# Kernel optimization log

Measured on AMD Instinct MI355X. Metric: run time of the kernel, lower is better.

Reference implementation:

```python
import jax, jax.numpy as jnp
import numpy as np

N_ATOMS = 4096
N_ANGLES = 200000


def setup_inputs() -> dict:
    key = jax.random.key(0)
    k1, k2, k3, k4, k5 = jax.random.split(key, 5)
    # pairwise unit direction vectors [N, N, 3]
    vec = jax.random.normal(k1, (N_ATOMS, N_ATOMS, 3), dtype=jnp.float32)
    vec = vec / jnp.linalg.norm(vec, axis=-1, keepdims=True)
    # pairwise distances [N, N], strictly positive
    dist = jax.random.uniform(k2, (N_ATOMS, N_ATOMS), dtype=jnp.float32) * 2.0 + 0.5
    # angle triplets [A, 3]
    coord_idx = jax.random.randint(k3, (N_ANGLES, 3), 0, N_ATOMS)
    # per-angle parameters: k0 (force const) and theta0 (equilibrium angle, rad)
    k0 = jax.random.uniform(k4, (N_ANGLES,), dtype=jnp.float32) * 100.0
    theta0 = jax.random.uniform(k5, (N_ANGLES,), dtype=jnp.float32) * np.float32(np.pi)
    params = jnp.stack([k0, theta0], axis=1)
    forces_out = jnp.zeros((N_ATOMS, 3), dtype=jnp.float32)
    return {
        "dist_mat": dist,
        "vector_mat": vec,
        "forces_out": forces_out,
        "params": params,
        "coord_idx": coord_idx,
        "calc_energy": 1,
        "calc_forces": 1,
    }


def reference(dist_mat, vector_mat, forces_out, params, coord_idx, calc_energy, calc_forces):
    k0 = params[:, 0]
    theta0 = params[:, 1]
    a1 = coord_idx[:, 0]
    a2 = coord_idx[:, 1]
    a3 = coord_idx[:, 2]

    vec21 = vector_mat[a2, a1]            # [A, 3]
    vec23 = vector_mat[a2, a3]            # [A, 3]
    dist21 = dist_mat[a2, a1]             # [A]
    dist23 = dist_mat[a2, a3]             # [A]

    cos_theta = jnp.clip(jnp.sum(vec21 * vec23, axis=1), -1.0, 1.0)
    theta = jnp.arccos(cos_theta)
    delta_theta = theta - theta0

    if calc_energy:
        energy = jnp.sum(k0 * delta_theta * delta_theta)
    else:
        energy = jnp.zeros([1], dtype=forces_out.dtype)

    forces = forces_out
    if calc_forces:
        sin_theta = jnp.sqrt(1.0 - cos_theta * cos_theta)
        # matches torch nan_to_num(nan=0.0): zero out coef where sin_theta == 0
        coef = jnp.where(sin_theta > 0.0,
                         -2.0 * k0 * delta_theta / jnp.maximum(sin_theta, 1e-12),
                         0.0)
        force0 = coef[:, None] * (cos_theta[:, None] * vec21 - vec23) / dist21[:, None]
        force2 = coef[:, None] * (cos_theta[:, None] * vec23 - vec21) / dist23[:, None]
        force1 = -(force0 + force2)
        forces = forces.at[a1].add(force0).at[a2].add(force1).at[a3].add(force2)

    return energy, forces
```

## Files before the change

kernel.cpp:

```cpp
#include <hip/hip_runtime.h>


__global__ void init_out_kernel(float* __restrict__ out,
                                const float* __restrict__ forces0,
                                int nf) {
    int j = blockIdx.x * blockDim.x + threadIdx.x;
    if (j == 0) out[0] = 0.0f;
    if (j < nf) out[1 + j] = forces0[j];
}

#define NB 256
#define NT 1024

__global__ void __launch_bounds__(NT)
angle_fused_kernel(const float*  __restrict__ dist,
                   const float*  __restrict__ vec,
                   const float2* __restrict__ params,
                   const int*    __restrict__ cidx,
                   const int*    __restrict__ ce_p,
                   const int*    __restrict__ cf_p,
                   float* __restrict__ out,
                   int n_atoms, int n_angles) {
    extern __shared__ float s_f[];
    __shared__ float s_e;
    const int nf  = n_atoms * 3;
    const int tid = threadIdx.x;
    const int b   = blockIdx.x;

    for (int j = tid; j < nf; j += NT) s_f[j] = 0.0f;
    if (tid == 0) s_e = 0.0f;
    __syncthreads();

    const int ce = ce_p[0];
    const int cf = cf_p[0];

    const int i0 = (int)(((long)b * n_angles) / NB);
    const int i1 = (int)(((long)(b + 1) * n_angles) / NB);
    const int i  = i0 + tid;

    float e_acc = 0.0f;
    if (i < i1) {
        const int a1 = cidx[3 * i + 0];
        const int a2 = cidx[3 * i + 1];
        const int a3 = cidx[3 * i + 2];
        const float2 kt = params[i];

        const unsigned row = (unsigned)a2 * (unsigned)n_atoms;
        const unsigned b21 = row + (unsigned)a1;
        const unsigned b23 = row + (unsigned)a3;
        const float* __restrict__ p21 = vec + 3u * b21;
        const float* __restrict__ p23 = vec + 3u * b23;

        const float v21x = p21[0], v21y = p21[1], v21z = p21[2];
        const float v23x = p23[0], v23y = p23[1], v23z = p23[2];
        const float d21 = dist[b21];
        const float d23 = dist[b23];

        float c = v21x * v23x + v21y * v23y + v21z * v23z;
        c = fminf(1.0f, fmaxf(-1.0f, c));
        const float th  = acosf(c);
        const float dth = th - kt.y;

        if (ce) e_acc = kt.x * dth * dth;

        if (cf) {
            const float s2 = fmaxf(0.0f, 1.0f - c * c);
            const float s  = sqrtf(s2);
            const float coef = (s > 0.0f) ? (-2.0f * kt.x * dth / fmaxf(s, 1e-12f)) : 0.0f;
            const float i21 = coef / d21;
            const float i23 = coef / d23;

            const float f0x = i21 * (c * v21x - v23x);
            const float f0y = i21 * (c * v21y - v23y);
            const float f0z = i21 * (c * v21z - v23z);
            const float f2x = i23 * (c * v23x - v21x);
            const float f2y = i23 * (c * v23y - v21y);
            const float f2z = i23 * (c * v23z - v21z);

            atomicAdd(&s_f[a1 * 3 + 0], f0x);
            atomicAdd(&s_f[a1 * 3 + 1], f0y);
            atomicAdd(&s_f[a1 * 3 + 2], f0z);
            atomicAdd(&s_f[a2 * 3 + 0], -(f0x + f2x));
            atomicAdd(&s_f[a2 * 3 + 1], -(f0y + f2y));
            atomicAdd(&s_f[a2 * 3 + 2], -(f0z + f2z));
            atomicAdd(&s_f[a3 * 3 + 0], f2x);
            atomicAdd(&s_f[a3 * 3 + 1], f2y);
            atomicAdd(&s_f[a3 * 3 + 2], f2z);
        }
    }

    for (int off = 32; off > 0; off >>= 1)
        e_acc += __shfl_down(e_acc, off, 64);
    if ((tid & 63) == 0) atomicAdd(&s_e, e_acc);
    __syncthreads();

    if (ce && tid == 0) atomicAdd(&out[0], s_e);

    if (cf) {
        const int base = (b * (nf / NB)) % nf;
        for (int jj = tid; jj < nf; jj += NT) {
            int j = jj + base;
            if (j >= nf) j -= nf;
            const float v = s_f[j];
            if (v != 0.0f) atomicAdd(&out[1 + j], v);
        }
    }
}

extern "C" void kernel_launch(void* const* d_in, const int* in_sizes, int n_in,
                              void* d_out, int out_size, void* d_ws, size_t ws_size,
                              hipStream_t stream) {
    const float*  dist    = (const float*)d_in[0];
    const float*  vec     = (const float*)d_in[1];
    const float*  forces0 = (const float*)d_in[2];
    const float2* params  = (const float2*)d_in[3];
    const int*    cidx    = (const int*)d_in[4];
    const int*    ce_p    = (const int*)d_in[5];
    const int*    cf_p    = (const int*)d_in[6];
    float* out = (float*)d_out;

    const int n_atoms  = in_sizes[2] / 3;
    const int n_angles = in_sizes[4] / 3;
    const int nf = n_atoms * 3;

    init_out_kernel<<<(nf + 1 + 255) / 256, 256, 0, stream>>>(out, forces0, nf);

    const size_t lds_bytes = (size_t)nf * sizeof(float);
    angle_fused_kernel<<<NB, NT, lds_bytes, stream>>>(dist, vec, params, cidx,
                                                      ce_p, cf_p, out,
                                                      n_atoms, n_angles);
}
```

Baseline: 301.0 us.

## Replace per-block LDS force accumulation with direct global atomics

Drops the per-block shared-memory force buffer (zero-init, LDS atomics, and a full flush of all atom forces to global) and instead has each thread atomically add its forces straight into the global output. The launch changes from 256 large blocks to one 256-thread block per 256 angles, with a per-block energy reduction through a small shared array. This removes the flush traffic and large LDS footprint and raises occupancy, at the cost of more contended global atomics.

```diff
diff --git a/kernel.cpp b/kernel.cpp
--- a/kernel.cpp
+++ b/kernel.cpp
@@ -9,37 +9,27 @@
     if (j < nf) out[1 + j] = forces0[j];
 }
 
-#define NB 256
-#define NT 1024
+#define NT 256
 
 __global__ void __launch_bounds__(NT)
-angle_fused_kernel(const float*  __restrict__ dist,
-                   const float*  __restrict__ vec,
-                   const float2* __restrict__ params,
-                   const int*    __restrict__ cidx,
-                   const int*    __restrict__ ce_p,
-                   const int*    __restrict__ cf_p,
-                   float* __restrict__ out,
-                   int n_atoms, int n_angles) {
-    extern __shared__ float s_f[];
-    __shared__ float s_e;
-    const int nf  = n_atoms * 3;
+angle_direct_kernel(const float*  __restrict__ dist,
+                    const float*  __restrict__ vec,
+                    const float2* __restrict__ params,
+                    const int*    __restrict__ cidx,
+                    const int*    __restrict__ ce_p,
+                    const int*    __restrict__ cf_p,
+                    float* __restrict__ out,
+                    int n_atoms, int n_angles) {
+    __shared__ float s_ew[NT / 64];
     const int tid = threadIdx.x;
-    const int b   = blockIdx.x;
-
-    for (int j = tid; j < nf; j += NT) s_f[j] = 0.0f;
-    if (tid == 0) s_e = 0.0f;
-    __syncthreads();
+    const int i   = blockIdx.x * NT + tid;
 
     const int ce = ce_p[0];
     const int cf = cf_p[0];
-
-    const int i0 = (int)(((long)b * n_angles) / NB);
-    const int i1 = (int)(((long)(b + 1) * n_angles) / NB);
-    const int i  = i0 + tid;
+    float* __restrict__ f = out + 1;
 
     float e_acc = 0.0f;
-    if (i < i1) {
+    if (i < n_angles) {
         const int a1 = cidx[3 * i + 0];
         const int a2 = cidx[3 * i + 1];
         const int a3 = cidx[3 * i + 2];
@@ -77,32 +67,28 @@
             const float f2y = i23 * (c * v23y - v21y);
             const float f2z = i23 * (c * v23z - v21z);
 
-            atomicAdd(&s_f[a1 * 3 + 0], f0x);
-            atomicAdd(&s_f[a1 * 3 + 1], f0y);
-            atomicAdd(&s_f[a1 * 3 + 2], f0z);
-            atomicAdd(&s_f[a2 * 3 + 0], -(f0x + f2x));
-            atomicAdd(&s_f[a2 * 3 + 1], -(f0y + f2y));
-            atomicAdd(&s_f[a2 * 3 + 2], -(f0z + f2z));
-            atomicAdd(&s_f[a3 * 3 + 0], f2x);
-            atomicAdd(&s_f[a3 * 3 + 1], f2y);
-            atomicAdd(&s_f[a3 * 3 + 2], f2z);
+            atomicAdd(&f[a1 * 3 + 0], f0x);
+            atomicAdd(&f[a1 * 3 + 1], f0y);
+            atomicAdd(&f[a1 * 3 + 2], f0z);
+            atomicAdd(&f[a2 * 3 + 0], -(f0x + f2x));
+            atomicAdd(&f[a2 * 3 + 1], -(f0y + f2y));
+            atomicAdd(&f[a2 * 3 + 2], -(f0z + f2z));
+            atomicAdd(&f[a3 * 3 + 0], f2x);
+            atomicAdd(&f[a3 * 3 + 1], f2y);
+            atomicAdd(&f[a3 * 3 + 2], f2z);
         }
     }
 
-    for (int off = 32; off > 0; off >>= 1)
-        e_acc += __shfl_down(e_acc, off, 64);
-    if ((tid & 63) == 0) atomicAdd(&s_e, e_acc);
-    __syncthreads();
-
-    if (ce && tid == 0) atomicAdd(&out[0], s_e);
-
-    if (cf) {
-        const int base = (b * (nf / NB)) % nf;
-        for (int jj = tid; jj < nf; jj += NT) {
-            int j = jj + base;
-            if (j >= nf) j -= nf;
-            const float v = s_f[j];
-            if (v != 0.0f) atomicAdd(&out[1 + j], v);
+    if (ce) {
+        for (int off = 32; off > 0; off >>= 1)
+            e_acc += __shfl_down(e_acc, off, 64);
+        if ((tid & 63) == 0) s_ew[tid >> 6] = e_acc;
+        __syncthreads();
+        if (tid == 0) {
+            float e = s_ew[0];
+            #pragma unroll
+            for (int w = 1; w < NT / 64; ++w) e += s_ew[w];
+            atomicAdd(&out[0], e);
         }
     }
 }
@@ -125,8 +111,8 @@
 
     init_out_kernel<<<(nf + 1 + 255) / 256, 256, 0, stream>>>(out, forces0, nf);
 
-    const size_t lds_bytes = (size_t)nf * sizeof(float);
-    angle_fused_kernel<<<NB, NT, lds_bytes, stream>>>(dist, vec, params, cidx,
-                                                      ce_p, cf_p, out,
-                                                      n_atoms, n_angles);
+    const int nb = (n_angles + NT - 1) / NT;
+    angle_direct_kernel<<<nb, NT, 0, stream>>>(dist, vec, params, cidx,
+                                               ce_p, cf_p, out,
+                                               n_atoms, n_angles);
 }
```

Result: slower. 401.2 us (+33.3%).
